# Optimization experiments

Measured on AMD Instinct MI355X. Metric: run time of the kernel, lower is better.

## Reference

```python
import jax, jax.numpy as jnp
import numpy as np

BN_EPS = 1e-5


def conv1d_reflect(x, w, dilation, bias=None):
    # x: [N, C_in, L], w: [C_out, C_in, K]; reflect pad preserves length for K=3, pad=dilation
    k = w.shape[-1]
    p = ((k - 1) * dilation + 1) // 2
    xp = jnp.pad(x, ((0, 0), (0, 0), (p, p)), mode='reflect')
    y = jax.lax.conv_general_dilated(
        xp, w, window_strides=(1,), padding='VALID',
        rhs_dilation=(dilation,), dimension_numbers=('NCH', 'OIH', 'NCH'))
    if bias is not None:
        y = y + bias[None, :, None]
    return y


def bn_eval(x, gamma, beta, mean, var):
    inv = gamma / jnp.sqrt(var + BN_EPS)
    return x * inv[None, :, None] + (beta - mean * inv)[None, :, None]


def upsample2_linear(x):
    # F.interpolate(scale_factor=2, mode='linear', align_corners=False)
    L = x.shape[-1]
    src = (jnp.arange(2 * L, dtype=jnp.float32) + 0.5) * 0.5 - 0.5
    src = jnp.maximum(src, 0.0)
    i0 = jnp.floor(src).astype(jnp.int32)
    i1 = jnp.minimum(i0 + 1, L - 1)
    w = (src - i0.astype(jnp.float32)).astype(x.dtype)
    return x[..., i0] * (1.0 - w) + x[..., i1] * w


def setup_inputs() -> dict:
    key = jax.random.key(0)
    ks = jax.random.split(key, 6)
    bt, st, ch, nt = 16, 4, 512, 1024
    fusion = jax.random.normal(ks[0], (bt, st, ch, nt), dtype=jnp.float32)
    targets = jax.random.uniform(ks[1], (bt, 3, 4 * nt, st), dtype=jnp.float32)
    c1, c2 = 256, 32
    w1 = jax.random.normal(ks[2], (c1, ch, 3), dtype=jnp.float32) * 0.05
    w2 = jax.random.normal(ks[3], (c2, c1, 3), dtype=jnp.float32) * 0.05
    w_out = jax.random.normal(ks[4], (3, c2, 3), dtype=jnp.float32) * 0.05
    b_out = jnp.zeros((3,), dtype=jnp.float32)
    return {
        'fusion': fusion, 'targets': targets,
        'w1': w1,
        'bn1_gamma': jnp.ones((c1,), jnp.float32), 'bn1_beta': jnp.zeros((c1,), jnp.float32),
        'bn1_mean': jnp.zeros((c1,), jnp.float32), 'bn1_var': jnp.ones((c1,), jnp.float32),
        'w2': w2,
        'bn2_gamma': jnp.ones((c2,), jnp.float32), 'bn2_beta': jnp.zeros((c2,), jnp.float32),
        'bn2_mean': jnp.zeros((c2,), jnp.float32), 'bn2_var': jnp.ones((c2,), jnp.float32),
        'w_out': w_out, 'b_out': b_out,
    }


def reference(fusion, targets, w1, bn1_gamma, bn1_beta, bn1_mean, bn1_var,
              w2, bn2_gamma, bn2_beta, bn2_mean, bn2_var, w_out, b_out):
    bt, st, ch, nt = fusion.shape
    x = fusion.reshape(bt * st, ch, nt)
    x = jax.nn.relu(bn_eval(conv1d_reflect(x, w1, dilation=8), bn1_gamma, bn1_beta, bn1_mean, bn1_var))
    x = upsample2_linear(x)
    x = jax.nn.relu(bn_eval(conv1d_reflect(x, w2, dilation=16), bn2_gamma, bn2_beta, bn2_mean, bn2_var))
    x = upsample2_linear(x)
    x = conv1d_reflect(x, w_out, dilation=32, bias=b_out)
    x = x.reshape(bt, st, x.shape[1], x.shape[2])
    x = jnp.transpose(x, (0, 2, 3, 1))  # [bt, 3, 4*nt, st]

    # losses: vectorized masked CE (replaces the python double loop)
    logp = jax.nn.log_softmax(x.astype(jnp.float32), axis=1)
    valid = jnp.any(targets != 0, axis=(1, 2))  # [bt, st]
    num = jnp.sum(valid).astype(jnp.float32)
    T = targets.shape[2]
    loss = jnp.sum(-targets * logp) / (num * T)
    return x, loss
```

## Files before the change

### kernel.cpp

```cpp
#include <hip/hip_runtime.h>
#include <hip/hip_bf16.h>

#define DEV static __device__ __forceinline__

typedef short bf16x8_t __attribute__((ext_vector_type(8)));
typedef float f32x4 __attribute__((ext_vector_type(4)));

#define GLDS16(gp, lp) __builtin_amdgcn_global_load_lds( \
    (const __attribute__((address_space(1))) void*)(gp), \
    (__attribute__((address_space(3))) void*)(lp), 16, 0, 0)

DEV int reflect_idx(int q, int L) {
    q = q < 0 ? -q : q;
    q = q >= L ? 2 * L - 2 - q : q;
    return q;
}

DEV unsigned short f2bf(float f) {
    unsigned int b = __float_as_uint(f);
    unsigned int r = (b + 0x7FFFu + ((b >> 16) & 1u)) >> 16;
    return (unsigned short)r;
}
DEV float bf2f(unsigned short u) {
    return __uint_as_float(((unsigned int)u) << 16);
}

__global__ void k0_init(float* lacc) {
    if (threadIdx.x < 8) lacc[threadIdx.x] = 0.0f;
}

__global__ void kw1b(const float* __restrict__ w1, unsigned short* __restrict__ wb) {
    int idx = blockIdx.x * 256 + threadIdx.x;
    int kk = idx >> 17;
    int rem = idx & 131071;
    int co = rem >> 9;
    int ci = rem & 511;
    wb[idx] = f2bf(w1[(co * 512 + ci) * 3 + kk]);
}

__global__ void kw2b(const float* __restrict__ w2, unsigned short* __restrict__ w2b) {
    int idx = blockIdx.x * 256 + threadIdx.x;
    int ci = idx & 255;
    int co = (idx >> 8) & 31;
    int kk = idx >> 13;
    w2b[idx] = f2bf(w2[(co * 256 + ci) * 3 + kk]);
}

__global__ __launch_bounds__(256) void kx_t(const float* __restrict__ x,
                                            unsigned short* __restrict__ xb, int n0) {
    __shared__ float ls[64][65];
    const int tid = threadIdx.x;
    const int t0 = blockIdx.x * 64, ci0 = blockIdx.y * 64;
    const int n = n0 + blockIdx.z;
    const float* xp = x + ((size_t)n * 512 + ci0) * 1024 + t0;
    for (int idx = tid; idx < 1024; idx += 256) {
        int r = idx >> 4, c4 = (idx & 15) * 4;
        float4 v = *(const float4*)(xp + r * 1024 + c4);
        ls[r][c4] = v.x; ls[r][c4 + 1] = v.y; ls[r][c4 + 2] = v.z; ls[r][c4 + 3] = v.w;
    }
    __syncthreads();
    unsigned short* xo = xb + ((size_t)blockIdx.z * 1024 + t0) * 512 + ci0;
#pragma unroll
    for (int p = 0; p < 2; ++p) {
        int trow = (tid >> 3) + p * 32;
        int cj = (tid & 7) * 8;
        unsigned short pk[8];
#pragma unroll
        for (int j = 0; j < 8; ++j) pk[j] = f2bf(ls[cj + j][trow]);
        *(uint4*)(xo + (size_t)trow * 512 + cj) = *(const uint4*)pk;
    }
}

__global__ __launch_bounds__(256, 2) void k1_mfma(
    const unsigned short* __restrict__ xb, const unsigned short* __restrict__ wb,
    const float* __restrict__ g, const float* __restrict__ be,
    const float* __restrict__ mn, const float* __restrict__ vr,
    unsigned short* __restrict__ y1t, int n0)
{
    const int tid  = threadIdx.x;
    const int lane = tid & 63;
    const int w    = tid >> 6;
    const int tw   = w >> 1;
    const int cw   = w & 1;
    const int tq   = lane & 15;
    const int qd   = lane >> 4;
    const int t0   = blockIdx.x * 128;
    const int nr   = blockIdx.y;
    const int n    = n0 + nr;
    const int cb   = blockIdx.z;

    __shared__ unsigned short smem[17408];

    const int rl0 = tid >> 2;
    const int rl1 = 64 + (tid >> 2);
    const int q0  = (tid & 3) ^ ((rl0 >> 1) & 3);
    const int q1  = (tid & 3) ^ ((rl1 >> 1) & 3);

    const unsigned short* xn = xb + (size_t)nr * 1024 * 512;
    int aoff0[3], aoff1[3];
#pragma unroll
    for (int kk = 0; kk < 3; ++kk) {
        aoff0[kk] = reflect_idx(t0 + rl0 + 8 * kk - 8, 1024) * 512 + q0 * 8;
        aoff1[kk] = reflect_idx(t0 + rl1 + 8 * kk - 8, 1024) * 512 + q1 * 8;
    }
    const unsigned short* wp0 = wb + (size_t)(cb * 128 + rl0) * 512 + q0 * 8;
    const unsigned short* wp1 = wb + (size_t)(cb * 128 + rl1) * 512 + q1 * 8;

    const int atom = qd ^ ((tq >> 1) & 3);

    f32x4 acc[4][4];
#pragma unroll
    for (int a = 0; a < 4; ++a)
#pragma unroll
        for (int b = 0; b < 4; ++b) acc[a][b] = (f32x4){0.f, 0.f, 0.f, 0.f};

    GLDS16(xn + aoff0[0], &smem[tid * 8]);
    GLDS16(xn + aoff1[0], &smem[2048 + tid * 8]);
    GLDS16(wp0, &smem[4096 + tid * 8]);
    GLDS16(wp1, &smem[6144 + tid * 8]);

#pragma unroll
    for (int c = 0; c < 48; ++c) {
        const int par = c & 1;
        __syncthreads();
        if (c < 47) {
            const int nc = c + 1, nk = nc >> 4, nj = nc & 15;
            const int bo = (par ^ 1) * 8192;
            GLDS16(xn + aoff0[nk] + nj * 32, &smem[bo + tid * 8]);
            GLDS16(xn + aoff1[nk] + nj * 32, &smem[bo + 2048 + tid * 8]);
            GLDS16(wp0 + (size_t)nk * 131072 + nj * 32, &smem[bo + 4096 + tid * 8]);
            GLDS16(wp1 + (size_t)nk * 131072 + nj * 32, &smem[bo + 6144 + tid * 8]);
        }
        const int ab = par * 8192;
        const int bb = par * 8192 + 4096;
        bf16x8_t Af[4], Bf[4];
#pragma unroll
        for (int ts = 0; ts < 4; ++ts)
            Af[ts] = *(const bf16x8_t*)&smem[ab + (tw * 64 + ts * 16 + tq) * 32 + atom * 8];
#pragma unroll
        for (int cs = 0; cs < 4; ++cs)
            Bf[cs] = *(const bf16x8_t*)&smem[bb + (cw * 64 + cs * 16 + tq) * 32 + atom * 8];
#pragma unroll
        for (int ts = 0; ts < 4; ++ts)
#pragma unroll
            for (int cs = 0; cs < 4; ++cs)
                acc[ts][cs] = __builtin_amdgcn_mfma_f32_16x16x32_bf16(
                    Af[ts], Bf[cs], acc[ts][cs], 0, 0, 0);
    }

    __syncthreads();
#pragma unroll
    for (int cs = 0; cs < 4; ++cs) {
        int col = cw * 64 + cs * 16 + tq;
        int co  = cb * 128 + col;
        float iv = g[co] / sqrtf(vr[co] + 1e-5f);
        float sh = be[co] - mn[co] * iv;
#pragma unroll
        for (int ts = 0; ts < 4; ++ts)
#pragma unroll
            for (int rg = 0; rg < 4; ++rg)
                smem[(tw * 64 + ts * 16 + qd * 4 + rg) * 136 + col] =
                    f2bf(fmaxf(fmaf(acc[ts][cs][rg], iv, sh), 0.0f));
    }
    __syncthreads();
    const int srow = tid >> 4, sseg = tid & 15;
#pragma unroll
    for (int p = 0; p < 8; ++p) {
        int row = p * 16 + srow;
        unsigned short* yp = y1t + ((size_t)n * 1024 + t0 + row) * 256 + cb * 128 + sseg * 8;
        *(uint4*)yp = *(const uint4*)&smem[row * 136 + sseg * 8];
    }
}

__global__ __launch_bounds__(256, 2) void k2_mfma(
    const unsigned short* __restrict__ y1t, const unsigned short* __restrict__ w2b,
    const float* __restrict__ g, const float* __restrict__ be,
    const float* __restrict__ mn, const float* __restrict__ vr,
    float* __restrict__ y2t)
{
    const int tid  = threadIdx.x;
    const int lane = tid & 63;
    const int w    = tid >> 6;
    const int tq   = lane & 15;
    const int qd   = lane >> 4;
    const int t0   = blockIdx.x * 256;
    const int n    = blockIdx.y;

    __shared__ union SM {
        unsigned short us[288 * 40];
        float tr[256 * 36];
    } sm;

    f32x4 acc[4][2];
#pragma unroll
    for (int a = 0; a < 4; ++a)
#pragma unroll
        for (int b = 0; b < 2; ++b) acc[a][b] = (f32x4){0.f, 0.f, 0.f, 0.f};

    const unsigned short* yn = y1t + (size_t)n * 1024 * 256;

    for (int ch = 0; ch < 8; ++ch) {
        const int ci0 = ch * 32;
        __syncthreads();
        for (int idx = tid; idx < 1152; idx += 256) {
            int r = idx >> 2, gq = idx & 3;
            int u = reflect_idx(t0 - 16 + r, 2048);
            float src = fmaxf((float)u * 0.5f - 0.25f, 0.0f);
            int i0 = (int)src;
            float wl = src - (float)i0;
            int i1 = i0 + 1 > 1023 ? 1023 : i0 + 1;
            const unsigned short* p0 = yn + (size_t)i0 * 256 + ci0 + gq * 8;
            const unsigned short* p1 = yn + (size_t)i1 * 256 + ci0 + gq * 8;
            uint4 ua = *(const uint4*)p0;
            uint4 ub = *(const uint4*)p1;
            const unsigned short* sa = (const unsigned short*)&ua;
            const unsigned short* sb = (const unsigned short*)&ub;
            unsigned short pk[8];
#pragma unroll
            for (int j = 0; j < 8; ++j) {
                float a = bf2f(sa[j]);
                float b = bf2f(sb[j]);
                pk[j] = f2bf(a + wl * (b - a));
            }
            *(uint4*)&sm.us[r * 40 + gq * 8] = *(const uint4*)pk;
        }
        __syncthreads();

        bf16x8_t Bf[2][3];
#pragma unroll
        for (int cs = 0; cs < 2; ++cs)
#pragma unroll
            for (int kk = 0; kk < 3; ++kk)
                Bf[cs][kk] = *(const bf16x8_t*)(w2b +
                    ((size_t)(kk * 32 + cs * 16 + tq)) * 256 + ci0 + qd * 8);

        bf16x8_t Af[6];
#pragma unroll
        for (int s = 0; s < 6; ++s)
            Af[s] = *(const bf16x8_t*)&sm.us[(w * 64 + s * 16 + tq) * 40 + qd * 8];

#pragma unroll
        for (int ts = 0; ts < 4; ++ts)
#pragma unroll
            for (int cs = 0; cs < 2; ++cs)
#pragma unroll
                for (int kk = 0; kk < 3; ++kk)
                    acc[ts][cs] = __builtin_amdgcn_mfma_f32_16x16x32_bf16(
                        Af[ts + kk], Bf[cs][kk], acc[ts][cs], 0, 0, 0);
    }

    __syncthreads();
#pragma unroll
    for (int cs = 0; cs < 2; ++cs) {
        int co = cs * 16 + tq;
        float iv = g[co] / sqrtf(vr[co] + 1e-5f);
        float sh = be[co] - mn[co] * iv;
#pragma unroll
        for (int ts = 0; ts < 4; ++ts)
#pragma unroll
            for (int rg = 0; rg < 4; ++rg) {
                int tl = w * 64 + ts * 16 + qd * 4 + rg;
                sm.tr[tl * 36 + co] = fmaxf(fmaf(acc[ts][cs][rg], iv, sh), 0.0f);
            }
    }
    __syncthreads();
    float* yo = y2t + ((size_t)n * 2048 + t0 + tid) * 32;
#pragma unroll
    for (int j = 0; j < 8; ++j)
        *(float4*)(yo + j * 4) = *(const float4*)&sm.tr[tid * 36 + j * 4];
}

__global__ __launch_bounds__(256, 2) void k3_out(
    const float* __restrict__ y2t, const float* __restrict__ w3,
    const float* __restrict__ bias, float* __restrict__ out)
{
    const int tid = threadIdx.x;
    const int t0 = blockIdx.x * 256;
    const int n  = blockIdx.y;

    __shared__ float us[32 * 321];
    __shared__ float wsh[288];

    for (int idx = tid; idx < 288; idx += 256) wsh[idx] = w3[idx];

    const float* yn = y2t + (size_t)n * 2048 * 32;
    for (int idx = tid; idx < 1280; idx += 256) {
        int r = idx >> 2, gq = idx & 3;
        int u = reflect_idx(t0 - 32 + r, 4096);
        float src = fmaxf((float)u * 0.5f - 0.25f, 0.0f);
        int i0 = (int)src;
        float wl = src - (float)i0;
        int i1 = i0 + 1 > 2047 ? 2047 : i0 + 1;
        const float* p0 = yn + (size_t)i0 * 32 + gq * 8;
        const float* p1 = yn + (size_t)i1 * 32 + gq * 8;
        float4 a0 = *(const float4*)p0;
        float4 a1 = *(const float4*)(p0 + 4);
        float4 b0 = *(const float4*)p1;
        float4 b1 = *(const float4*)(p1 + 4);
        float v[8];
        v[0] = a0.x + wl * (b0.x - a0.x); v[1] = a0.y + wl * (b0.y - a0.y);
        v[2] = a0.z + wl * (b0.z - a0.z); v[3] = a0.w + wl * (b0.w - a0.w);
        v[4] = a1.x + wl * (b1.x - a1.x); v[5] = a1.y + wl * (b1.y - a1.y);
        v[6] = a1.z + wl * (b1.z - a1.z); v[7] = a1.w + wl * (b1.w - a1.w);
#pragma unroll
        for (int j = 0; j < 8; ++j)
            us[(gq * 8 + j) * 321 + r] = v[j];
    }
    __syncthreads();

    float a0 = 0.0f, a1 = 0.0f, a2 = 0.0f;
#pragma unroll 8
    for (int ci = 0; ci < 32; ++ci) {
        float x0 = us[ci * 321 + tid];
        float x1 = us[ci * 321 + tid + 32];
        float x2 = us[ci * 321 + tid + 64];
        a0 = fmaf(wsh[(0 * 32 + ci) * 3 + 0], x0, a0);
        a0 = fmaf(wsh[(0 * 32 + ci) * 3 + 1], x1, a0);
        a0 = fmaf(wsh[(0 * 32 + ci) * 3 + 2], x2, a0);
        a1 = fmaf(wsh[(1 * 32 + ci) * 3 + 0], x0, a1);
        a1 = fmaf(wsh[(1 * 32 + ci) * 3 + 1], x1, a1);
        a1 = fmaf(wsh[(1 * 32 + ci) * 3 + 2], x2, a1);
        a2 = fmaf(wsh[(2 * 32 + ci) * 3 + 0], x0, a2);
        a2 = fmaf(wsh[(2 * 32 + ci) * 3 + 1], x1, a2);
        a2 = fmaf(wsh[(2 * 32 + ci) * 3 + 2], x2, a2);
    }
    int b = n >> 2, s = n & 3;
    int t = t0 + tid;
    size_t ob = ((size_t)(b * 3) * 4096 + t) * 4 + s;
    out[ob]         = a0 + bias[0];
    out[ob + 16384] = a1 + bias[1];
    out[ob + 32768] = a2 + bias[2];
}

__global__ void k4a_valid(const float* __restrict__ tg, float* lacc) {
    __shared__ int flag;
    if (threadIdx.x == 0) flag = 0;
    __syncthreads();
    int b = blockIdx.x >> 2, s = blockIdx.x & 3;
    bool any = false;
    for (int idx = threadIdx.x; idx < 3 * 4096; idx += 256) {
        int c = idx >> 12, t = idx & 4095;
        float v = tg[((size_t)(b * 3 + c) * 4096 + t) * 4 + s];
        any |= (v != 0.0f);
    }
    if (any) flag = 1;
    __syncthreads();
    if (threadIdx.x == 0 && flag) atomicAdd((int*)(lacc + 1), 1);
}

__global__ __launch_bounds__(256) void k4b_ce(
    const float* __restrict__ x, const float* __restrict__ tg, float* lacc)
{
    int i = blockIdx.x * 256 + threadIdx.x;
    int s = i & 3;
    int t = (i >> 2) & 4095;
    int b = i >> 14;
    size_t base = ((size_t)(b * 3) * 4096 + t) * 4 + s;
    float x0 = x[base], x1 = x[base + 16384], x2 = x[base + 32768];
    float mx = fmaxf(x0, fmaxf(x1, x2));
    float e0 = expf(x0 - mx), e1 = expf(x1 - mx), e2 = expf(x2 - mx);
    float lse = mx + logf(e0 + e1 + e2);
    float g0 = tg[base], g1 = tg[base + 16384], g2 = tg[base + 32768];
    float v = g0 * (lse - x0) + g1 * (lse - x1) + g2 * (lse - x2);

    for (int off = 32; off > 0; off >>= 1) v += __shfl_down(v, off);
    __shared__ float wsum[4];
    int lane = threadIdx.x & 63, wid = threadIdx.x >> 6;
    if (lane == 0) wsum[wid] = v;
    __syncthreads();
    if (threadIdx.x == 0) {
        atomicAdd(lacc, wsum[0] + wsum[1] + wsum[2] + wsum[3]);
    }
}

__global__ void k4c_final(const float* lacc, float* out) {
    if (threadIdx.x == 0) {
        float sum = lacc[0];
        int num = ((const int*)lacc)[1];
        out[786432] = sum / ((float)num * 4096.0f);
    }
}

extern "C" void kernel_launch(void* const* d_in, const int* in_sizes, int n_in,
                              void* d_out, int out_size, void* d_ws, size_t ws_size,
                              hipStream_t stream) {
    (void)in_sizes; (void)n_in; (void)out_size;
    const float* fusion  = (const float*)d_in[0];
    const float* targets = (const float*)d_in[1];
    const float* w1  = (const float*)d_in[2];
    const float* g1  = (const float*)d_in[3];
    const float* be1 = (const float*)d_in[4];
    const float* mn1 = (const float*)d_in[5];
    const float* vr1 = (const float*)d_in[6];
    const float* w2  = (const float*)d_in[7];
    const float* g2  = (const float*)d_in[8];
    const float* be2 = (const float*)d_in[9];
    const float* mn2 = (const float*)d_in[10];
    const float* vr2 = (const float*)d_in[11];
    const float* w3  = (const float*)d_in[12];
    const float* b3  = (const float*)d_in[13];
    float* out = (float*)d_out;

    char* ws = (char*)d_ws;
    unsigned short* y1t = (unsigned short*)ws;
    unsigned short* xb  = (unsigned short*)(ws + 33554432);
    float* y2t = (float*)(ws + 33554432);

    const bool single = ws_size >= 101500000ull;
    size_t woff = single ? (33554432ull + 67108864ull) : (33554432ull + 16777216ull);
    unsigned short* wb  = (unsigned short*)(ws + woff);
    unsigned short* w2b = (unsigned short*)(ws + woff + 786432);
    float* lacc = (float*)(ws + woff + 786432 + 49152);

    k0_init<<<1, 64, 0, stream>>>(lacc);
    kw1b<<<1536, 256, 0, stream>>>(w1, wb);
    kw2b<<<96, 256, 0, stream>>>(w2, w2b);
    if (single) {
        kx_t<<<dim3(16, 8, 64), 256, 0, stream>>>(fusion, xb, 0);
        k1_mfma<<<dim3(8, 64, 2), 256, 0, stream>>>(xb, wb, g1, be1, mn1, vr1, y1t, 0);
    } else {
        for (int r = 0; r < 4; ++r) {
            kx_t<<<dim3(16, 8, 16), 256, 0, stream>>>(fusion, xb, r * 16);
            k1_mfma<<<dim3(8, 16, 2), 256, 0, stream>>>(xb, wb, g1, be1, mn1, vr1, y1t, r * 16);
        }
    }
    k2_mfma<<<dim3(8, 64), 256, 0, stream>>>(y1t, w2b, g2, be2, mn2, vr2, y2t);
    k3_out<<<dim3(16, 64), 256, 0, stream>>>(y2t, w3, b3, out);
    k4a_valid<<<64, 256, 0, stream>>>(targets, lacc);
    k4b_ce<<<1024, 256, 0, stream>>>(out, targets, lacc);
    k4c_final<<<1, 64, 0, stream>>>(lacc, out);
}
```

Baseline: 376.0 us.

## Deepen k1 K-chunks, double-buffer k2 staging, fuse prep and validity kernels

k1 now loads two 32-wide K slices per stage, which halves the barrier count and doubles LDS use to 64KB. k2 double-buffers its interpolated input tile so the next channel chunk is staged while the current one computes. The weight conversion and accumulator init are merged into a single prep kernel. The separate target-validity scan is folded into the CE kernel through per-(b,s) atomicOr flags. The larger LDS footprint may limit k1 occupancy, and the atomicOr flags add atomics in k4b.

```diff
diff --git a/kernel.cpp b/kernel.cpp
--- a/kernel.cpp
+++ b/kernel.cpp
@@ -25,25 +25,24 @@
     return __uint_as_float(((unsigned int)u) << 16);
 }
 
-__global__ void k0_init(float* lacc) {
-    if (threadIdx.x < 8) lacc[threadIdx.x] = 0.0f;
-}
-
-__global__ void kw1b(const float* __restrict__ w1, unsigned short* __restrict__ wb) {
+__global__ void kprep(const float* __restrict__ w1, const float* __restrict__ w2,
+                      unsigned short* __restrict__ wb, unsigned short* __restrict__ w2b,
+                      float* lacc) {
     int idx = blockIdx.x * 256 + threadIdx.x;
-    int kk = idx >> 17;
-    int rem = idx & 131071;
-    int co = rem >> 9;
-    int ci = rem & 511;
-    wb[idx] = f2bf(w1[(co * 512 + ci) * 3 + kk]);
-}
-
-__global__ void kw2b(const float* __restrict__ w2, unsigned short* __restrict__ w2b) {
-    int idx = blockIdx.x * 256 + threadIdx.x;
-    int ci = idx & 255;
-    int co = (idx >> 8) & 31;
-    int kk = idx >> 13;
-    w2b[idx] = f2bf(w2[(co * 256 + ci) * 3 + kk]);
+    if (idx < 393216) {
+        int kk = idx >> 17;
+        int rem = idx & 131071;
+        int co = rem >> 9;
+        int ci = rem & 511;
+        wb[idx] = f2bf(w1[(co * 512 + ci) * 3 + kk]);
+    } else if (idx < 417792) {
+        int j = idx - 393216;
+        int ci = j & 255;
+        int co = (j >> 8) & 31;
+        int kk = j >> 13;
+        w2b[j] = f2bf(w2[(co * 256 + ci) * 3 + kk]);
+    }
+    if (idx < 128) lacc[idx] = 0.0f;
 }
 
 __global__ __launch_bounds__(256) void kx_t(const float* __restrict__ x,
@@ -89,7 +88,7 @@
     const int n    = n0 + nr;
     const int cb   = blockIdx.z;
 
-    __shared__ unsigned short smem[17408];
+    __shared__ unsigned short smem[32768];
 
     const int rl0 = tid >> 2;
     const int rl1 = 64 + (tid >> 2);
@@ -114,38 +113,47 @@
 #pragma unroll
         for (int b = 0; b < 4; ++b) acc[a][b] = (f32x4){0.f, 0.f, 0.f, 0.f};
 
-    GLDS16(xn + aoff0[0], &smem[tid * 8]);
-    GLDS16(xn + aoff1[0], &smem[2048 + tid * 8]);
-    GLDS16(wp0, &smem[4096 + tid * 8]);
-    GLDS16(wp1, &smem[6144 + tid * 8]);
-
-#pragma unroll
-    for (int c = 0; c < 48; ++c) {
-        const int par = c & 1;
+#pragma unroll
+    for (int p = 0; p < 2; ++p) {
+        GLDS16(xn + aoff0[0] + p * 32, &smem[p * 8192 + tid * 8]);
+        GLDS16(xn + aoff1[0] + p * 32, &smem[p * 8192 + 2048 + tid * 8]);
+        GLDS16(wp0 + p * 32, &smem[p * 8192 + 4096 + tid * 8]);
+        GLDS16(wp1 + p * 32, &smem[p * 8192 + 6144 + tid * 8]);
+    }
+
+#pragma unroll
+    for (int c = 0; c < 24; ++c) {
+        const int bo = (c & 1) * 16384;
         __syncthreads();
-        if (c < 47) {
-            const int nc = c + 1, nk = nc >> 4, nj = nc & 15;
-            const int bo = (par ^ 1) * 8192;
-            GLDS16(xn + aoff0[nk] + nj * 32, &smem[bo + tid * 8]);
-            GLDS16(xn + aoff1[nk] + nj * 32, &smem[bo + 2048 + tid * 8]);
-            GLDS16(wp0 + (size_t)nk * 131072 + nj * 32, &smem[bo + 4096 + tid * 8]);
-            GLDS16(wp1 + (size_t)nk * 131072 + nj * 32, &smem[bo + 6144 + tid * 8]);
+        if (c < 23) {
+            const int nc = c + 1, nk = nc >> 3, nj = nc & 7;
+            const int no = ((c + 1) & 1) * 16384;
+#pragma unroll
+            for (int p = 0; p < 2; ++p) {
+                const int col = nj * 64 + p * 32;
+                GLDS16(xn + aoff0[nk] + col, &smem[no + p * 8192 + tid * 8]);
+                GLDS16(xn + aoff1[nk] + col, &smem[no + p * 8192 + 2048 + tid * 8]);
+                GLDS16(wp0 + (size_t)nk * 131072 + col, &smem[no + p * 8192 + 4096 + tid * 8]);
+                GLDS16(wp1 + (size_t)nk * 131072 + col, &smem[no + p * 8192 + 6144 + tid * 8]);
+            }
         }
-        const int ab = par * 8192;
-        const int bb = par * 8192 + 4096;
-        bf16x8_t Af[4], Bf[4];
-#pragma unroll
-        for (int ts = 0; ts < 4; ++ts)
-            Af[ts] = *(const bf16x8_t*)&smem[ab + (tw * 64 + ts * 16 + tq) * 32 + atom * 8];
-#pragma unroll
-        for (int cs = 0; cs < 4; ++cs)
-            Bf[cs] = *(const bf16x8_t*)&smem[bb + (cw * 64 + cs * 16 + tq) * 32 + atom * 8];
-#pragma unroll
-        for (int ts = 0; ts < 4; ++ts)
+#pragma unroll
+        for (int p = 0; p < 2; ++p) {
+            const int ab = bo + p * 8192;
+            bf16x8_t Af[4], Bf[4];
+#pragma unroll
+            for (int ts = 0; ts < 4; ++ts)
+                Af[ts] = *(const bf16x8_t*)&smem[ab + (tw * 64 + ts * 16 + tq) * 32 + atom * 8];
 #pragma unroll
             for (int cs = 0; cs < 4; ++cs)
-                acc[ts][cs] = __builtin_amdgcn_mfma_f32_16x16x32_bf16(
-                    Af[ts], Bf[cs], acc[ts][cs], 0, 0, 0);
+                Bf[cs] = *(const bf16x8_t*)&smem[ab + 4096 + (cw * 64 + cs * 16 + tq) * 32 + atom * 8];
+#pragma unroll
+            for (int ts = 0; ts < 4; ++ts)
+#pragma unroll
+                for (int cs = 0; cs < 4; ++cs)
+                    acc[ts][cs] = __builtin_amdgcn_mfma_f32_16x16x32_bf16(
+                        Af[ts], Bf[cs], acc[ts][cs], 0, 0, 0);
+        }
     }
 
     __syncthreads();
@@ -187,7 +195,7 @@
     const int n    = blockIdx.y;
 
     __shared__ union SM {
-        unsigned short us[288 * 40];
+        unsigned short us[2][288 * 40];
         float tr[256 * 36];
     } sm;
 
@@ -199,9 +207,8 @@
 
     const unsigned short* yn = y1t + (size_t)n * 1024 * 256;
 
-    for (int ch = 0; ch < 8; ++ch) {
+    auto stage = [&](int ch, int buf) {
         const int ci0 = ch * 32;
-        __syncthreads();
         for (int idx = tid; idx < 1152; idx += 256) {
             int r = idx >> 2, gq = idx & 3;
             int u = reflect_idx(t0 - 16 + r, 2048);
@@ -222,10 +229,17 @@
                 float b = bf2f(sb[j]);
                 pk[j] = f2bf(a + wl * (b - a));
             }
-            *(uint4*)&sm.us[r * 40 + gq * 8] = *(const uint4*)pk;
+            *(uint4*)&sm.us[buf][r * 40 + gq * 8] = *(const uint4*)pk;
         }
+    };
+
+    stage(0, 0);
+    for (int ch = 0; ch < 8; ++ch) {
+        const int buf = ch & 1;
         __syncthreads();
-
+        if (ch < 7) stage(ch + 1, buf ^ 1);
+
+        const int ci0 = ch * 32;
         bf16x8_t Bf[2][3];
 #pragma unroll
         for (int cs = 0; cs < 2; ++cs)
@@ -237,7 +251,7 @@
         bf16x8_t Af[6];
 #pragma unroll
         for (int s = 0; s < 6; ++s)
-            Af[s] = *(const bf16x8_t*)&sm.us[(w * 64 + s * 16 + tq) * 40 + qd * 8];
+            Af[s] = *(const bf16x8_t*)&sm.us[buf][(w * 64 + s * 16 + tq) * 40 + qd * 8];
 
 #pragma unroll
         for (int ts = 0; ts < 4; ++ts)
@@ -332,22 +346,6 @@
     out[ob + 32768] = a2 + bias[2];
 }
 
-__global__ void k4a_valid(const float* __restrict__ tg, float* lacc) {
-    __shared__ int flag;
-    if (threadIdx.x == 0) flag = 0;
-    __syncthreads();
-    int b = blockIdx.x >> 2, s = blockIdx.x & 3;
-    bool any = false;
-    for (int idx = threadIdx.x; idx < 3 * 4096; idx += 256) {
-        int c = idx >> 12, t = idx & 4095;
-        float v = tg[((size_t)(b * 3 + c) * 4096 + t) * 4 + s];
-        any |= (v != 0.0f);
-    }
-    if (any) flag = 1;
-    __syncthreads();
-    if (threadIdx.x == 0 && flag) atomicAdd((int*)(lacc + 1), 1);
-}
-
 __global__ __launch_bounds__(256) void k4b_ce(
     const float* __restrict__ x, const float* __restrict__ tg, float* lacc)
 {
@@ -362,21 +360,31 @@
     float lse = mx + logf(e0 + e1 + e2);
     float g0 = tg[base], g1 = tg[base + 16384], g2 = tg[base + 32768];
     float v = g0 * (lse - x0) + g1 * (lse - x1) + g2 * (lse - x2);
+    bool nz = (g0 != 0.0f) | (g1 != 0.0f) | (g2 != 0.0f);
+
+    __shared__ float wsum[4];
+    __shared__ int sf[4];
+    if (threadIdx.x < 4) sf[threadIdx.x] = 0;
+    __syncthreads();
+    if (nz) sf[s] = 1;
 
     for (int off = 32; off > 0; off >>= 1) v += __shfl_down(v, off);
-    __shared__ float wsum[4];
     int lane = threadIdx.x & 63, wid = threadIdx.x >> 6;
     if (lane == 0) wsum[wid] = v;
     __syncthreads();
-    if (threadIdx.x == 0) {
+    if (threadIdx.x == 0)
         atomicAdd(lacc, wsum[0] + wsum[1] + wsum[2] + wsum[3]);
-    }
+    if (threadIdx.x < 4 && sf[threadIdx.x])
+        atomicOr((int*)lacc + 8 + b * 4 + threadIdx.x, 1);
 }
 
 __global__ void k4c_final(const float* lacc, float* out) {
     if (threadIdx.x == 0) {
         float sum = lacc[0];
-        int num = ((const int*)lacc)[1];
+        const int* vf = (const int*)lacc + 8;
+        int num = 0;
+#pragma unroll
+        for (int j = 0; j < 64; ++j) num += (vf[j] != 0);
         out[786432] = sum / ((float)num * 4096.0f);
     }
 }
@@ -412,9 +420,7 @@
     unsigned short* w2b = (unsigned short*)(ws + woff + 786432);
     float* lacc = (float*)(ws + woff + 786432 + 49152);
 
-    k0_init<<<1, 64, 0, stream>>>(lacc);
-    kw1b<<<1536, 256, 0, stream>>>(w1, wb);
-    kw2b<<<96, 256, 0, stream>>>(w2, w2b);
+    kprep<<<1632, 256, 0, stream>>>(w1, w2, wb, w2b, lacc);
     if (single) {
         kx_t<<<dim3(16, 8, 64), 256, 0, stream>>>(fusion, xb, 0);
         k1_mfma<<<dim3(8, 64, 2), 256, 0, stream>>>(xb, wb, g1, be1, mn1, vr1, y1t, 0);
@@ -426,7 +432,6 @@
     }
     k2_mfma<<<dim3(8, 64), 256, 0, stream>>>(y1t, w2b, g2, be2, mn2, vr2, y2t);
     k3_out<<<dim3(16, 64), 256, 0, stream>>>(y2t, w3, b3, out);
-    k4a_valid<<<64, 256, 0, stream>>>(targets, lacc);
     k4b_ce<<<1024, 256, 0, stream>>>(out, targets, lacc);
     k4c_final<<<1, 64, 0, stream>>>(lacc, out);
 }
```

Result: faster. 359.9 us (-4.3%).
